# Performance work log

Hardware: AMD Instinct MI355X
Metric: run time of the kernel (lower is better)

## Reference

```python
import jax, jax.numpy as jnp
import numpy as np

HID = 256


def setup_inputs() -> dict:
    key0 = jax.random.key(0)
    ks = jax.random.split(key0, 6)
    bsz, m, Lq, Lk = 8, 16, 64, 2048
    query = jax.random.normal(ks[0], (bsz, Lq, HID), dtype=jnp.float32)
    key = jax.random.normal(ks[1], (bsz * m, Lk, HID), dtype=jnp.float32)
    # nn.Linear params (weight is [out, in]); init scale ~ 1/sqrt(fan_in)
    s = 1.0 / np.sqrt(HID)
    w_q = jax.random.uniform(ks[2], (HID, HID), jnp.float32, -s, s)
    b_q = jax.random.uniform(ks[3], (HID,), jnp.float32, -s, s)
    w_k = jax.random.uniform(ks[4], (HID, HID), jnp.float32, -s, s)
    b_k = jax.random.uniform(ks[5], (HID,), jnp.float32, -s, s)
    return {"query": query, "key": key, "w_q": w_q, "b_q": b_q, "w_k": w_k, "b_k": b_k}


def reference(query, key, w_q, b_q, w_k, b_k):
    bsz = query.shape[0]
    msz = key.shape[0]
    m = msz // bsz
    hid = query.shape[-1]
    scale = jnp.sqrt(jnp.float32(hid))
    Q = jnp.einsum("bqh,oh->bqo", query, w_q) + b_q            # [b, Lq, h]
    K = jnp.einsum("nkh,oh->nko", key, w_k) + b_k              # [b*m, Lk, h]
    K = K.reshape(bsz, m, -1, hid)                               # [b, m, Lk, h]
    key_r = key.reshape(bsz, m, -1, hid)                         # [b, m, Lk, h]
    # energy[b,m,q,k] = Q[b,q,:] . K[b,m,k,:] / sqrt(hid)
    energy = jnp.einsum("bqh,bmkh->bmqk", Q, K) / scale         # [b, m, Lq, Lk]
    total_attention = jnp.sum(energy, axis=-2)                   # [b, m, Lk]
    attention = jnp.mean(total_attention, axis=-1)               # [b, m]
    max_index = jnp.argmax(attention, axis=-1)                   # [b]
    # gather the raw key block for the best candidate per batch item
    val = jnp.take_along_axis(key_r, max_index[:, None, None, None], axis=1)
    return val[:, 0]                                             # [b, Lk, h]
```

## Files before the change

### kernel.cpp

```cpp
#include <hip/hip_runtime.h>

#define HID 256
#define LK  2048
#define LQ  64
#define BSZ 8
#define M   16
#define NKEY (BSZ * M)

__global__ void colsum_kernel(const float* __restrict__ query,
                              const float* __restrict__ key,
                              float* __restrict__ partial,
                              float* __restrict__ qsum,
                              int split) {
    const int bid  = blockIdx.x;
    const int t    = threadIdx.x;
    const int wave = t >> 6;
    const int lane = t & 63;
    const int nK   = NKEY * split;

    const float* base;
    float* dst;
    int rows;
    if (bid < nK) {
        const int n = bid / split, chunk = bid % split;
        rows = LK / split;
        base = key + (size_t)n * LK * HID + (size_t)chunk * rows * HID;
        dst  = partial + (size_t)bid * HID;
    } else {
        const int b = bid - nK;
        rows = LQ;
        base = query + (size_t)b * LQ * HID;
        dst  = qsum + (size_t)b * HID;
    }

    float4 acc = make_float4(0.f, 0.f, 0.f, 0.f);
    for (int r = wave; r < rows; r += 4) {
        float4 v = ((const float4*)(base + (size_t)r * HID))[lane];
        acc.x += v.x; acc.y += v.y; acc.z += v.z; acc.w += v.w;
    }

    __shared__ float lds[4][HID];
    ((float4*)lds[wave])[lane] = acc;
    __syncthreads();
    float s = lds[0][t] + lds[1][t] + lds[2][t] + lds[3][t];
    dst[t] = s;
}

__global__ void project_kernel(const float* __restrict__ partial,
                               const float* __restrict__ qsum,
                               const float* __restrict__ w_q,
                               const float* __restrict__ b_q,
                               const float* __restrict__ w_k,
                               const float* __restrict__ b_k,
                               float* __restrict__ ksv,
                               float* __restrict__ qsv,
                               int split) {
    __shared__ float sred[HID];
    const int bid = blockIdx.x;
    const int t   = threadIdx.x;

    const float* W;
    const float* bias;
    float lfac;
    float* dst;
    if (bid < NKEY) {
        float s = 0.f;
        for (int c = 0; c < split; ++c)
            s += partial[((size_t)bid * split + c) * HID + t];
        sred[t] = s;
        W = w_k; bias = b_k; lfac = (float)LK; dst = ksv + (size_t)bid * HID;
    } else {
        const int b = bid - NKEY;
        sred[t] = qsum[(size_t)b * HID + t];
        W = w_q; bias = b_q; lfac = (float)LQ; dst = qsv + (size_t)b * HID;
    }
    __syncthreads();

    const float4* Wrow = (const float4*)(W + (size_t)t * HID);
    float acc = 0.f;
#pragma unroll 8
    for (int h4 = 0; h4 < HID / 4; ++h4) {
        float4 w = Wrow[h4];
        acc += w.x * sred[h4 * 4 + 0] + w.y * sred[h4 * 4 + 1]
             + w.z * sred[h4 * 4 + 2] + w.w * sred[h4 * 4 + 3];
    }
    dst[t] = acc + lfac * bias[t];
}

__global__ void argmax_kernel(const float* __restrict__ ksv,
                              const float* __restrict__ qsv,
                              int* __restrict__ idx) {
    const int b    = blockIdx.x;
    const int t    = threadIdx.x;
    const int wave = t >> 6;
    const int lane = t & 63;

    __shared__ float att[M];
    __shared__ float wpart[4];

    const float q = qsv[(size_t)b * HID + t];
    for (int m = 0; m < M; ++m) {
        float v = q * ksv[((size_t)b * M + m) * HID + t];
        for (int off = 32; off; off >>= 1) v += __shfl_down(v, off);
        if (lane == 0) wpart[wave] = v;
        __syncthreads();
        if (t == 0) att[m] = wpart[0] + wpart[1] + wpart[2] + wpart[3];
        __syncthreads();
    }
    if (t == 0) {
        int best = 0;
        float bv = att[0];
        for (int m = 1; m < M; ++m)
            if (att[m] > bv) { bv = att[m]; best = m; }
        idx[b] = best;
    }
}

__global__ void gather_kernel(const float* __restrict__ key,
                              const int* __restrict__ idx,
                              float* __restrict__ out) {
    const size_t per_b = (size_t)LK * HID / 4;
    const size_t i = (size_t)blockIdx.x * blockDim.x + threadIdx.x;
    const int b = (int)(i / per_b);
    const size_t off = i % per_b;
    const int n = b * M + idx[b];
    ((float4*)out)[i] = ((const float4*)key)[(size_t)n * per_b + off];
}

extern "C" void kernel_launch(void* const* d_in, const int* in_sizes, int n_in,
                              void* d_out, int out_size, void* d_ws, size_t ws_size,
                              hipStream_t stream) {
    const float* query = (const float*)d_in[0];
    const float* key   = (const float*)d_in[1];
    const float* w_q   = (const float*)d_in[2];
    const float* b_q   = (const float*)d_in[3];
    const float* w_k   = (const float*)d_in[4];
    const float* b_k   = (const float*)d_in[5];
    float* out = (float*)d_out;

    int split = 16;
    while (split > 1) {
        size_t need = sizeof(float) * ((size_t)NKEY * split * HID
                                       + (size_t)BSZ * HID
                                       + (size_t)NKEY * HID
                                       + (size_t)BSZ * HID)
                      + sizeof(int) * BSZ;
        if (need <= ws_size) break;
        split >>= 1;
    }

    float* ws = (float*)d_ws;
    size_t off = 0;
    float* partial = ws + off; off += (size_t)NKEY * split * HID;
    float* qsum    = ws + off; off += (size_t)BSZ * HID;
    float* ksv     = ws + off; off += (size_t)NKEY * HID;
    float* qsv     = ws + off; off += (size_t)BSZ * HID;
    int*   idx     = (int*)(ws + off);

    const int nColBlocks = NKEY * split + BSZ;
    hipLaunchKernelGGL(colsum_kernel, dim3(nColBlocks), dim3(256), 0, stream,
                       query, key, partial, qsum, split);

    hipLaunchKernelGGL(project_kernel, dim3(NKEY + BSZ), dim3(256), 0, stream,
                       partial, qsum, w_q, b_q, w_k, b_k, ksv, qsv, split);

    hipLaunchKernelGGL(argmax_kernel, dim3(BSZ), dim3(256), 0, stream,
                       ksv, qsv, idx);

    const int nGatherBlocks = (int)((size_t)BSZ * LK * HID / 4 / 256);
    hipLaunchKernelGGL(gather_kernel, dim3(nGatherBlocks), dim3(256), 0, stream,
                       key, idx, out);
}
```

Baseline: 79.92 us.

## Fold key projection into query-side vector and drop the projection kernel

The energy score is rewritten as u·colsum(key), where u = W_kᵀ(W_q·sum(query) + Lq·b_q). The key-bias term is dropped because it adds the same value to every candidate and cannot change the argmax. This removes the separate projection kernel and its 128 GEMV blocks, so colsum blocks now compute u on the side and argmax reduces the split partials directly. Split is also raised to 32, the colsum loop uses contiguous per-wave row ranges with two accumulators, and gather uses a 2D grid to avoid per-thread division. The trade-offs are more partials for argmax to sum and a reduction order that differs slightly from before.

```diff
diff --git a/kernel.cpp b/kernel.cpp
--- a/kernel.cpp
+++ b/kernel.cpp
@@ -9,87 +9,70 @@
 
 __global__ void colsum_kernel(const float* __restrict__ query,
                               const float* __restrict__ key,
+                              const float* __restrict__ w_q,
+                              const float* __restrict__ b_q,
+                              const float* __restrict__ w_k,
                               float* __restrict__ partial,
-                              float* __restrict__ qsum,
+                              float* __restrict__ u,
                               int split) {
-    const int bid  = blockIdx.x;
-    const int t    = threadIdx.x;
-    const int wave = t >> 6;
-    const int lane = t & 63;
-    const int nK   = NKEY * split;
-
-    const float* base;
-    float* dst;
-    int rows;
-    if (bid < nK) {
-        const int n = bid / split, chunk = bid % split;
-        rows = LK / split;
-        base = key + (size_t)n * LK * HID + (size_t)chunk * rows * HID;
-        dst  = partial + (size_t)bid * HID;
-    } else {
-        const int b = bid - nK;
-        rows = LQ;
-        base = query + (size_t)b * LQ * HID;
-        dst  = qsum + (size_t)b * HID;
-    }
-
-    float4 acc = make_float4(0.f, 0.f, 0.f, 0.f);
-    for (int r = wave; r < rows; r += 4) {
-        float4 v = ((const float4*)(base + (size_t)r * HID))[lane];
-        acc.x += v.x; acc.y += v.y; acc.z += v.z; acc.w += v.w;
-    }
-
-    __shared__ float lds[4][HID];
-    ((float4*)lds[wave])[lane] = acc;
-    __syncthreads();
-    float s = lds[0][t] + lds[1][t] + lds[2][t] + lds[3][t];
-    dst[t] = s;
-}
-
-__global__ void project_kernel(const float* __restrict__ partial,
-                               const float* __restrict__ qsum,
-                               const float* __restrict__ w_q,
-                               const float* __restrict__ b_q,
-                               const float* __restrict__ w_k,
-                               const float* __restrict__ b_k,
-                               float* __restrict__ ksv,
-                               float* __restrict__ qsv,
-                               int split) {
-    __shared__ float sred[HID];
     const int bid = blockIdx.x;
     const int t   = threadIdx.x;
 
-    const float* W;
-    const float* bias;
-    float lfac;
-    float* dst;
-    if (bid < NKEY) {
+    if (bid < BSZ) {
+        __shared__ float qs[HID];
+        __shared__ float qsv[HID];
+        const int b = bid;
+        const float* qbase = query + (size_t)b * LQ * HID;
         float s = 0.f;
-        for (int c = 0; c < split; ++c)
-            s += partial[((size_t)bid * split + c) * HID + t];
-        sred[t] = s;
-        W = w_k; bias = b_k; lfac = (float)LK; dst = ksv + (size_t)bid * HID;
+        for (int r = 0; r < LQ; ++r) s += qbase[(size_t)r * HID + t];
+        qs[t] = s;
+        __syncthreads();
+        const float4* wrow = (const float4*)(w_q + (size_t)t * HID);
+        float acc = 0.f;
+#pragma unroll 8
+        for (int h4 = 0; h4 < HID / 4; ++h4) {
+            float4 w = wrow[h4];
+            acc += w.x * qs[h4 * 4 + 0] + w.y * qs[h4 * 4 + 1]
+                 + w.z * qs[h4 * 4 + 2] + w.w * qs[h4 * 4 + 3];
+        }
+        qsv[t] = acc + (float)LQ * b_q[t];
+        __syncthreads();
+        float uh = 0.f;
+#pragma unroll 4
+        for (int o = 0; o < HID; ++o) uh += qsv[o] * w_k[(size_t)o * HID + t];
+        u[(size_t)b * HID + t] = uh;
     } else {
-        const int b = bid - NKEY;
-        sred[t] = qsum[(size_t)b * HID + t];
-        W = w_q; bias = b_q; lfac = (float)LQ; dst = qsv + (size_t)b * HID;
+        const int kb    = bid - BSZ;
+        const int n     = kb / split;
+        const int chunk = kb % split;
+        const int rows  = LK / split;
+        const float* base = key + (size_t)n * LK * HID + (size_t)chunk * rows * HID;
+        const int wave = t >> 6;
+        const int lane = t & 63;
+
+        float4 acc0 = make_float4(0.f, 0.f, 0.f, 0.f);
+        float4 acc1 = make_float4(0.f, 0.f, 0.f, 0.f);
+        const int r0 = wave * (rows / 4);
+#pragma unroll 4
+        for (int i = 0; i < rows / 4; i += 2) {
+            float4 v0 = ((const float4*)(base + (size_t)(r0 + i) * HID))[lane];
+            float4 v1 = ((const float4*)(base + (size_t)(r0 + i + 1) * HID))[lane];
+            acc0.x += v0.x; acc0.y += v0.y; acc0.z += v0.z; acc0.w += v0.w;
+            acc1.x += v1.x; acc1.y += v1.y; acc1.z += v1.z; acc1.w += v1.w;
+        }
+        acc0.x += acc1.x; acc0.y += acc1.y; acc0.z += acc1.z; acc0.w += acc1.w;
+
+        __shared__ float lds[4][HID];
+        ((float4*)lds[wave])[lane] = acc0;
+        __syncthreads();
+        partial[(size_t)kb * HID + t] = lds[0][t] + lds[1][t] + lds[2][t] + lds[3][t];
     }
-    __syncthreads();
-
-    const float4* Wrow = (const float4*)(W + (size_t)t * HID);
-    float acc = 0.f;
-#pragma unroll 8
-    for (int h4 = 0; h4 < HID / 4; ++h4) {
-        float4 w = Wrow[h4];
-        acc += w.x * sred[h4 * 4 + 0] + w.y * sred[h4 * 4 + 1]
-             + w.z * sred[h4 * 4 + 2] + w.w * sred[h4 * 4 + 3];
-    }
-    dst[t] = acc + lfac * bias[t];
 }
 
-__global__ void argmax_kernel(const float* __restrict__ ksv,
-                              const float* __restrict__ qsv,
-                              int* __restrict__ idx) {
+__global__ void argmax_kernel(const float* __restrict__ partial,
+                              const float* __restrict__ u,
+                              int* __restrict__ idx,
+                              int split) {
     const int b    = blockIdx.x;
     const int t    = threadIdx.x;
     const int wave = t >> 6;
@@ -98,9 +81,12 @@
     __shared__ float att[M];
     __shared__ float wpart[4];
 
-    const float q = qsv[(size_t)b * HID + t];
+    const float uv = u[(size_t)b * HID + t];
     for (int m = 0; m < M; ++m) {
-        float v = q * ksv[((size_t)b * M + m) * HID + t];
+        const float* p = partial + ((size_t)(b * M + m) * split) * HID + t;
+        float s = 0.f;
+        for (int c = 0; c < split; ++c) s += p[(size_t)c * HID];
+        float v = uv * s;
         for (int off = 32; off; off >>= 1) v += __shfl_down(v, off);
         if (lane == 0) wpart[wave] = v;
         __syncthreads();
@@ -119,12 +105,11 @@
 __global__ void gather_kernel(const float* __restrict__ key,
                               const int* __restrict__ idx,
                               float* __restrict__ out) {
+    const int b = blockIdx.y;
     const size_t per_b = (size_t)LK * HID / 4;
-    const size_t i = (size_t)blockIdx.x * blockDim.x + threadIdx.x;
-    const int b = (int)(i / per_b);
-    const size_t off = i % per_b;
+    const size_t off = (size_t)blockIdx.x * blockDim.x + threadIdx.x;
     const int n = b * M + idx[b];
-    ((float4*)out)[i] = ((const float4*)key)[(size_t)n * per_b + off];
+    ((float4*)out)[(size_t)b * per_b + off] = ((const float4*)key)[(size_t)n * per_b + off];
 }
 
 extern "C" void kernel_launch(void* const* d_in, const int* in_sizes, int n_in,
@@ -135,14 +120,11 @@
     const float* w_q   = (const float*)d_in[2];
     const float* b_q   = (const float*)d_in[3];
     const float* w_k   = (const float*)d_in[4];
-    const float* b_k   = (const float*)d_in[5];
     float* out = (float*)d_out;
 
-    int split = 16;
+    int split = 32;
     while (split > 1) {
         size_t need = sizeof(float) * ((size_t)NKEY * split * HID
-                                       + (size_t)BSZ * HID
-                                       + (size_t)NKEY * HID
                                        + (size_t)BSZ * HID)
                       + sizeof(int) * BSZ;
         if (need <= ws_size) break;
@@ -152,22 +134,16 @@
     float* ws = (float*)d_ws;
     size_t off = 0;
     float* partial = ws + off; off += (size_t)NKEY * split * HID;
-    float* qsum    = ws + off; off += (size_t)BSZ * HID;
-    float* ksv     = ws + off; off += (size_t)NKEY * HID;
-    float* qsv     = ws + off; off += (size_t)BSZ * HID;
+    float* u       = ws + off; off += (size_t)BSZ * HID;
     int*   idx     = (int*)(ws + off);
 
-    const int nColBlocks = NKEY * split + BSZ;
-    hipLaunchKernelGGL(colsum_kernel, dim3(nColBlocks), dim3(256), 0, stream,
-                       query, key, partial, qsum, split);
-
-    hipLaunchKernelGGL(project_kernel, dim3(NKEY + BSZ), dim3(256), 0, stream,
-                       partial, qsum, w_q, b_q, w_k, b_k, ksv, qsv, split);
+    const int nBlocks = BSZ + NKEY * split;
+    hipLaunchKernelGGL(colsum_kernel, dim3(nBlocks), dim3(256), 0, stream,
+                       query, key, w_q, b_q, w_k, partial, u, split);
 
     hipLaunchKernelGGL(argmax_kernel, dim3(BSZ), dim3(256), 0, stream,
-                       ksv, qsv, idx);
+                       partial, u, idx, split);
 
-    const int nGatherBlocks = (int)((size_t)BSZ * LK * HID / 4 / 256);
-    hipLaunchKernelGGL(gather_kernel, dim3(nGatherBlocks), dim3(256), 0, stream,
+    hipLaunchKernelGGL(gather_kernel, dim3(512, BSZ), dim3(256), 0, stream,
                        key, idx, out);
 }
```

New measurement: 190.3 us. 2.38x slower.
